# Kernel optimization log

Hardware: AMD Instinct MI355X
Metric: run time of the kernel (lower is better)

## Reference

```python
import jax, jax.numpy as jnp
import numpy as np

N_NODES = 100000
N_EDGES = 1600000
D_IN = 64
HID = 64


def setup_inputs() -> dict:
    key = jax.random.key(0)
    ks = jax.random.split(key, 8)
    s = 0.1  # modest weight scale
    return {
        "x": jax.random.normal(ks[0], (N_NODES, D_IN), jnp.float32),
        "edge_index": jax.random.randint(ks[1], (2, N_EDGES), 0, N_NODES),
        "W1": jax.random.normal(ks[2], (D_IN, HID), jnp.float32) * s,
        "b1": jnp.zeros((HID,), jnp.float32),
        "W2": jax.random.normal(ks[3], (HID, HID), jnp.float32) * s,
        "b2": jnp.zeros((HID,), jnp.float32),
        "fc1_w": jax.random.normal(ks[4], (HID, 256), jnp.float32) * s,
        "fc1_b": jnp.zeros((256,), jnp.float32),
        "fc2_w": jax.random.normal(ks[5], (256, 1), jnp.float32) * s,
        "fc2_b": jnp.zeros((1,), jnp.float32),
    }


def reference(x, edge_index, W1, b1, W2, b2, fc1_w, fc1_b, fc2_w, fc2_b):
    N = x.shape[0]
    loop = jnp.arange(N, dtype=edge_index.dtype)
    # GCNConv default: add self-loops + symmetric D^{-1/2}(A+I)D^{-1/2} normalization
    row = jnp.concatenate([edge_index[0], loop])  # source nodes
    col = jnp.concatenate([edge_index[1], loop])  # target nodes
    deg = jax.ops.segment_sum(jnp.ones(row.shape[0], x.dtype), col, num_segments=N)
    dinv = jnp.where(deg > 0, jax.lax.rsqrt(deg), 0.0)
    norm = dinv[row] * dinv[col]  # [E+N]

    def gcn_conv(h, W, b):
        h = h @ W                                   # [N, H] transform first
        msg = h[row] * norm[:, None]                # gather + scale, [E+N, H]
        return jax.ops.segment_sum(msg, col, num_segments=N) + b

    # dropout is inactive in eval mode (training=False)
    h = jax.nn.relu(gcn_conv(x, W1, b1))
    h = jax.nn.relu(gcn_conv(h, W2, b2))
    h = jax.nn.relu(h @ fc1_w + fc1_b)
    out = h @ fc2_w + fc2_b                          # [N, 1]
    # F.normalize(out, dim=0): L2 normalize along node dim, eps=1e-12
    out = out / jnp.maximum(jnp.sqrt(jnp.sum(out * out, axis=0, keepdims=True)), 1e-12)
    return out
```

## Files before the change

### kernel.cpp

```cpp
#include <hip/hip_runtime.h>
#include <hip/hip_bf16.h>

typedef unsigned short u16;
typedef unsigned int u32;
typedef __attribute__((ext_vector_type(8))) short short8;
typedef __attribute__((ext_vector_type(4))) float f32x4;

__device__ __forceinline__ float bf2f(u16 h) {
  return __uint_as_float(((u32)h) << 16);
}
__device__ __forceinline__ float ldconv(const void* p, int i, int fl) {
  return fl ? bf2f(((const u16*)p)[i]) : ((const float*)p)[i];
}
__device__ __forceinline__ u16 f2bf(float v) {
  __hip_bfloat16 h = __float2bfloat16(v);
  return *(u16*)&h;
}

__global__ void k_flag(const void* x, int* flag, float* ssum, int* bcnt) {
  __shared__ float red[256];
  int t = threadIdx.x;
  const u16* h = (const u16*)x;
  float m = 0.f;
  for (int i = t; i < 1024; i += 256) m = fmaxf(m, fabsf(bf2f(h[i])));
  red[t] = m; __syncthreads();
  for (int off = 128; off > 0; off >>= 1) {
    if (t < off) red[t] = fmaxf(red[t], red[t + off]);
    __syncthreads();
  }
  bcnt[t] = 0;
  if (t == 0) { *flag = (red[0] < 1000.0f) ? 1 : 0; *ssum = 0.f; }
}

__global__ void k_conv_w(const void* W1, const void* b1, const void* W2, const void* b2,
                         const void* f1w, const void* f1b, const void* f2w, const void* f2b,
                         u16* wbh, float* wbf, const int* flag) {
  int fl = *flag;
  int i = blockIdx.x * blockDim.x + threadIdx.x;
  if (i < 4096) {
    int n = i >> 6, k = i & 63;
    wbh[i] = f2bf(ldconv(W1, k * 64 + n, fl));
  } else if (i < 8192) {
    int j = i - 4096; int n = j >> 6, k = j & 63;
    wbh[i] = f2bf(ldconv(W2, k * 64 + n, fl));
  } else if (i < 24576) {
    int j = i - 8192; int n = j >> 6, k = j & 63;
    wbh[i] = f2bf(ldconv(f1w, k * 256 + n, fl));
  } else if (i < 24576 + 641) {
    int j = i - 24576;
    float v;
    if (j < 64)       v = ldconv(b1,  j,       fl);
    else if (j < 128) v = ldconv(b2,  j - 64,  fl);
    else if (j < 384) v = ldconv(f1b, j - 128, fl);
    else if (j < 640) v = ldconv(f2w, j - 384, fl);
    else              v = ldconv(f2b, 0,       fl);
    wbf[j] = v;
  }
}

__global__ __launch_bounds__(256) void k_bcount(const int* __restrict__ eidx, int E, int npb,
                                                int* bcnt) {
  __shared__ int hist[256];
  int t = threadIdx.x;
  hist[t] = 0;
  __syncthreads();
  int e0 = blockIdx.x * 8192;
  int e1 = min(e0 + 8192, E);
  for (int e = e0 + t; e < e1; e += 256) {
    int tgt = eidx[E + e];
    atomicAdd(&hist[tgt / npb], 1);
  }
  __syncthreads();
  if (hist[t]) atomicAdd(&bcnt[t], hist[t]);
}

__global__ void k_bscan(const int* __restrict__ bcnt, int* bbase, int* bcur) {
  __shared__ int tmp[256];
  int t = threadIdx.x;
  int v = bcnt[t];
  tmp[t] = v; __syncthreads();
  for (int off = 1; off < 256; off <<= 1) {
    int u = (t >= off) ? tmp[t - off] : 0;
    __syncthreads();
    tmp[t] += u;
    __syncthreads();
  }
  bbase[t] = tmp[t] - v;
  bcur[t]  = tmp[t] - v;
}

__global__ __launch_bounds__(256) void k_bfill(const int* __restrict__ eidx, int E, int npb,
                                               int* bcur, u32* bdata) {
  __shared__ int hist[256];
  __shared__ int base[256];
  int t = threadIdx.x;
  hist[t] = 0;
  __syncthreads();
  int e0 = blockIdx.x * 8192;
  int e1 = min(e0 + 8192, E);
  for (int e = e0 + t; e < e1; e += 256) {
    int tgt = eidx[E + e];
    atomicAdd(&hist[tgt / npb], 1);
  }
  __syncthreads();
  base[t] = hist[t] ? atomicAdd(&bcur[t], hist[t]) : 0;
  hist[t] = 0;
  __syncthreads();
  for (int e = e0 + t; e < e1; e += 256) {
    int src = eidx[e];
    int tgt = eidx[E + e];
    int b = tgt / npb;
    int idx = atomicAdd(&hist[b], 1);
    bdata[base[b] + idx] = ((u32)src << 9) | (u32)(tgt - b * npb);
  }
}

__global__ __launch_bounds__(256) void k_degb(const u32* __restrict__ bdata,
                                              const int* __restrict__ bbase,
                                              const int* __restrict__ bcnt,
                                              int* deg, int N, int npb) {
  __shared__ int hist[512];
  int b = blockIdx.x, t = threadIdx.x;
  int node0 = b * npb;
  if (node0 >= N) return;
  int ncnt = min(npb, N - node0);
  for (int j = t; j < 512; j += 256) hist[j] = 0;
  __syncthreads();
  int base = bbase[b], cnt = bcnt[b];
  for (int e = t; e < cnt; e += 256) atomicAdd(&hist[bdata[base + e] & 511], 1);
  __syncthreads();
  for (int j = t; j < ncnt; j += 256) deg[node0 + j] = hist[j] + 1;
}

__global__ void k_scan_a(const int* __restrict__ deg, int* csr_ptr, int* bsum, int N) {
  __shared__ int tmp[256];
  int t = threadIdx.x;
  int i = blockIdx.x * 256 + t;
  int c = (i < N) ? (deg[i] - 1) : 0;
  tmp[t] = c; __syncthreads();
  for (int off = 1; off < 256; off <<= 1) {
    int u = (t >= off) ? tmp[t - off] : 0;
    __syncthreads();
    tmp[t] += u;
    __syncthreads();
  }
  if (i < N) csr_ptr[i] = tmp[t] - c;
  if (t == 255) bsum[blockIdx.x] = tmp[255];
}

__global__ void k_scan_b(const int* __restrict__ bsum, int* bsum2, int G) {
  __shared__ int tmp[512];
  int t = threadIdx.x;
  int v = (t < G) ? bsum[t] : 0;
  tmp[t] = v; __syncthreads();
  for (int off = 1; off < 512; off <<= 1) {
    int u = (t >= off) ? tmp[t - off] : 0;
    __syncthreads();
    tmp[t] += u;
    __syncthreads();
  }
  if (t < G) bsum2[t] = tmp[t] - v;
}

__global__ void k_scan_c(int* csr_ptr, const int* __restrict__ bsum2,
                         const int* __restrict__ deg, float* dinv, int N) {
  int i = blockIdx.x * 256 + threadIdx.x;
  if (i >= N) return;
  csr_ptr[i] += bsum2[blockIdx.x];
  dinv[i] = 1.0f / sqrtf((float)deg[i]);
}

__global__ __launch_bounds__(256) void k_p2(const u32* __restrict__ bdata,
                                            const int* __restrict__ bbase,
                                            const int* __restrict__ bcnt,
                                            const int* __restrict__ csr_ptr,
                                            int* __restrict__ crow, int N, int npb, int E) {
  __shared__ int lds[8192];
  __shared__ int cur[512];
  int b = blockIdx.x, t = threadIdx.x;
  int node0 = b * npb;
  if (node0 >= N) return;
  int ncnt = min(npb, N - node0);
  int rs = csr_ptr[node0];
  int re = (node0 + ncnt < N) ? csr_ptr[node0 + ncnt] : E;
  for (int j = t; j < ncnt; j += 256) cur[j] = csr_ptr[node0 + j] - rs;
  __syncthreads();
  int base = bbase[b], cnt = bcnt[b];
  for (int e = t; e < cnt; e += 256) {
    u32 pk = bdata[base + e];
    int tl = pk & 511;
    int pos = atomicAdd(&cur[tl], 1);
    if (pos < 8192) lds[pos] = (int)(pk >> 9);
  }
  __syncthreads();
  int len = re - rs;
  for (int j = t; j < len; j += 256) crow[rs + j] = lds[j];
}

__global__ __launch_bounds__(256) void k_xform(const void* __restrict__ in, int inbf,
                                               const int* __restrict__ flagp,
                                               const u16* __restrict__ wT,
                                               const float* __restrict__ dinv,
                                               u16* __restrict__ out, int N) {
  __shared__ __align__(16) u16 ws[64 * 72];
  int t = threadIdx.x;
  #pragma unroll
  for (int f = t; f < 512; f += 256) {
    int n = f >> 3, o = f & 7;
    *(float4*)&ws[n * 72 + o * 8] = ((const float4*)wT)[f];
  }
  __syncthreads();
  int fl = inbf ? 1 : *flagp;
  int lane = t & 63, wid = t >> 6;
  int g = lane >> 4, c = lane & 15;
  int arow = blockIdx.x * 64 + wid * 16 + c;
  short8 a0 = {0, 0, 0, 0, 0, 0, 0, 0}, a1 = {0, 0, 0, 0, 0, 0, 0, 0};
  if (arow < N) {
    if (fl) {
      const u16* p = (const u16*)in + (size_t)arow * 64 + g * 8;
      a0 = *(const short8*)p;
      a1 = *(const short8*)(p + 32);
    } else {
      const float* p = (const float*)in + (size_t)arow * 64 + g * 8;
      u16 tmp[16];
      #pragma unroll
      for (int j = 0; j < 8; j++) tmp[j] = f2bf(p[j]);
      #pragma unroll
      for (int j = 0; j < 8; j++) tmp[8 + j] = f2bf(p[32 + j]);
      a0 = *(short8*)tmp;
      a1 = *(short8*)(tmp + 8);
    }
  }
  int rbase = blockIdx.x * 64 + wid * 16 + g * 4;
  float dv[4];
  #pragma unroll
  for (int r = 0; r < 4; r++) dv[r] = (rbase + r < N) ? dinv[rbase + r] : 0.f;
  #pragma unroll
  for (int tile = 0; tile < 4; tile++) {
    short8 b0 = *(const short8*)&ws[(tile * 16 + c) * 72 + g * 8];
    short8 b1 = *(const short8*)&ws[(tile * 16 + c) * 72 + g * 8 + 32];
    f32x4 z = {0.f, 0.f, 0.f, 0.f};
    f32x4 acc = __builtin_amdgcn_mfma_f32_16x16x32_bf16(a0, b0, z, 0, 0, 0);
    acc = __builtin_amdgcn_mfma_f32_16x16x32_bf16(a1, b1, acc, 0, 0, 0);
    #pragma unroll
    for (int r = 0; r < 4; r++) {
      int orow = rbase + r;
      if (orow < N) out[(size_t)orow * 64 + tile * 16 + c] = f2bf(acc[r] * dv[r]);
    }
  }
}

__global__ __launch_bounds__(256) void k_agg(const u16* __restrict__ src, u16* __restrict__ dst,
                                             const int* __restrict__ csr_row,
                                             const int* __restrict__ csr_ptr,
                                             const int* __restrict__ deg,
                                             const float* __restrict__ dinv,
                                             const float* __restrict__ bias, int N) {
  int lane = threadIdx.x & 63;
  int wid = threadIdx.x >> 6;
  int i = blockIdx.x * 4 + wid;
  if (i >= N) return;
  int sub = lane >> 4;
  int fq  = lane & 15;
  int start = csr_ptr[i];
  int total = deg[i];
  const u16* base = src + (size_t)fq * 4;
  float a0 = 0.f, a1 = 0.f, a2 = 0.f, a3 = 0.f;
  #pragma unroll 2
  for (int t = sub; t < total; t += 4) {
    int r = (t == 0) ? i : csr_row[start + t - 1];
    uint2 v = *(const uint2*)(base + (size_t)r * 64);
    a0 += __uint_as_float(v.x << 16);
    a1 += __uint_as_float(v.x & 0xffff0000u);
    a2 += __uint_as_float(v.y << 16);
    a3 += __uint_as_float(v.y & 0xffff0000u);
  }
  a0 += __shfl_xor(a0, 16); a1 += __shfl_xor(a1, 16);
  a2 += __shfl_xor(a2, 16); a3 += __shfl_xor(a3, 16);
  a0 += __shfl_xor(a0, 32); a1 += __shfl_xor(a1, 32);
  a2 += __shfl_xor(a2, 32); a3 += __shfl_xor(a3, 32);
  if (sub == 0) {
    float di = dinv[i];
    float4 b4 = ((const float4*)bias)[fq];
    u16 o[4];
    o[0] = f2bf(fmaxf(fmaf(a0, di, b4.x), 0.f));
    o[1] = f2bf(fmaxf(fmaf(a1, di, b4.y), 0.f));
    o[2] = f2bf(fmaxf(fmaf(a2, di, b4.z), 0.f));
    o[3] = f2bf(fmaxf(fmaf(a3, di, b4.w), 0.f));
    *(uint2*)&dst[(size_t)i * 64 + fq * 4] = *(uint2*)o;
  }
}

__global__ __launch_bounds__(256) void k_fc(const u16* __restrict__ h,
                                            const u16* __restrict__ fc1T,
                                            const float* __restrict__ wf,
                                            float* __restrict__ outf,
                                            float* __restrict__ ssum, int N) {
  __shared__ __align__(16) u16 ws[256 * 72];
  __shared__ float red[16];
  int t = threadIdx.x;
  #pragma unroll
  for (int f = t; f < 2048; f += 256) {
    int n = f >> 3, o = f & 7;
    *(float4*)&ws[n * 72 + o * 8] = ((const float4*)fc1T)[f];
  }
  __syncthreads();
  int lane = t & 63, wid = t >> 6;
  int g = lane >> 4, c = lane & 15;
  int arow = blockIdx.x * 64 + wid * 16 + c;
  short8 a0 = {0, 0, 0, 0, 0, 0, 0, 0}, a1 = {0, 0, 0, 0, 0, 0, 0, 0};
  if (arow < N) {
    a0 = *(const short8*)&h[(size_t)arow * 64 + g * 8];
    a1 = *(const short8*)&h[(size_t)arow * 64 + g * 8 + 32];
  }
  float psum[4] = {0.f, 0.f, 0.f, 0.f};
  #pragma unroll
  for (int tile = 0; tile < 16; tile++) {
    short8 b0 = *(const short8*)&ws[(tile * 16 + c) * 72 + g * 8];
    short8 b1 = *(const short8*)&ws[(tile * 16 + c) * 72 + g * 8 + 32];
    f32x4 z = {0.f, 0.f, 0.f, 0.f};
    f32x4 acc = __builtin_amdgcn_mfma_f32_16x16x32_bf16(a0, b0, z, 0, 0, 0);
    acc = __builtin_amdgcn_mfma_f32_16x16x32_bf16(a1, b1, acc, 0, 0, 0);
    int col = tile * 16 + c;
    float fb = wf[128 + col];
    float fw = wf[384 + col];
    #pragma unroll
    for (int r = 0; r < 4; r++) psum[r] += fmaxf(acc[r] + fb, 0.f) * fw;
  }
  #pragma unroll
  for (int off = 1; off < 16; off <<= 1) {
    #pragma unroll
    for (int r = 0; r < 4; r++) psum[r] += __shfl_xor(psum[r], off);
  }
  float fc2b = wf[640];
  if (c == 0) {
    float ss = 0.f;
    int rbase = blockIdx.x * 64 + wid * 16 + g * 4;
    #pragma unroll
    for (int r = 0; r < 4; r++) {
      int row = rbase + r;
      if (row < N) {
        float o = psum[r] + fc2b;
        outf[row] = o;
        ss += o * o;
      }
    }
    red[wid * 4 + g] = ss;
  }
  __syncthreads();
  if (t == 0) {
    float s = 0.f;
    #pragma unroll
    for (int j = 0; j < 16; j++) s += red[j];
    atomicAdd(ssum, s);
  }
}

__global__ void k_norm(const float* __restrict__ outf, const float* __restrict__ ssum,
                       void* dout, int N, const int* flag) {
  int i = blockIdx.x * blockDim.x + threadIdx.x;
  if (i >= N) return;
  float denom = fmaxf(sqrtf(*ssum), 1e-12f);
  float v = outf[i] / denom;
  if (*flag) ((__hip_bfloat16*)dout)[i] = __float2bfloat16(v);
  else       ((float*)dout)[i] = v;
}

extern "C" void kernel_launch(void* const* d_in, const int* in_sizes, int n_in,
                              void* d_out, int out_size, void* d_ws, size_t ws_size,
                              hipStream_t stream) {
  const void* x   = d_in[0];
  const int* eidx = (const int*)d_in[1];
  const void* W1  = d_in[2]; const void* b1  = d_in[3];
  const void* W2  = d_in[4]; const void* b2  = d_in[5];
  const void* f1w = d_in[6]; const void* f1b = d_in[7];
  const void* f2w = d_in[8]; const void* f2b = d_in[9];
  int N = in_sizes[0] / 64;
  int E = in_sizes[1] / 2;
  int npb = (N + 255) / 256;

  char* ws = (char*)d_ws;
  size_t off = 0;
  auto alloc = [&](size_t b) {
    void* p = ws + off;
    off = (off + b + 255) & ~(size_t)255;
    return p;
  };
  int*   flag  = (int*)  alloc(4);
  float* ssum  = (float*)alloc(4);
  int*   bcnt  = (int*)  alloc(256 * 4);
  int*   bbase = (int*)  alloc(256 * 4);
  int*   bcur  = (int*)  alloc(256 * 4);
  u32*   bdata = (u32*)  alloc((size_t)E * 4);
  int*   deg   = (int*)  alloc((size_t)N * 4);
  int*   ptr   = (int*)  alloc((size_t)N * 4);
  int*   bsum  = (int*)  alloc(512 * 4);
  int*   bsum2 = (int*)  alloc(512 * 4);
  float* dinv  = (float*)alloc((size_t)N * 4);
  int*   crow  = (int*)  alloc((size_t)E * 4);
  u16*   wbh   = (u16*)  alloc(24576 * 2);
  float* wbf   = (float*)alloc(641 * 4);
  u16*   HA    = (u16*)  alloc((size_t)N * 64 * 2);
  u16*   HT    = (u16*)  alloc((size_t)N * 64 * 2);
  float* outf  = (float*)alloc((size_t)N * 4);

  int GN = (N + 255) / 256;
  int GEB = (E + 8191) / 8192;
  int NT = (N + 63) / 64;

  k_flag<<<1, 256, 0, stream>>>(x, flag, ssum, bcnt);
  k_conv_w<<<(24576 + 641 + 255) / 256, 256, 0, stream>>>(W1, b1, W2, b2, f1w, f1b, f2w, f2b,
                                                          wbh, wbf, flag);
  k_bcount<<<GEB, 256, 0, stream>>>(eidx, E, npb, bcnt);
  k_bscan<<<1, 256, 0, stream>>>(bcnt, bbase, bcur);
  k_bfill<<<GEB, 256, 0, stream>>>(eidx, E, npb, bcur, bdata);
  k_degb<<<256, 256, 0, stream>>>(bdata, bbase, bcnt, deg, N, npb);
  k_scan_a<<<GN, 256, 0, stream>>>(deg, ptr, bsum, N);
  k_scan_b<<<1, 512, 0, stream>>>(bsum, bsum2, GN);
  k_scan_c<<<GN, 256, 0, stream>>>(ptr, bsum2, deg, dinv, N);
  k_p2<<<256, 256, 0, stream>>>(bdata, bbase, bcnt, ptr, crow, N, npb, E);

  k_xform<<<NT, 256, 0, stream>>>(x, 0, flag, wbh + 0, dinv, HT, N);
  k_agg<<<(N + 3) / 4, 256, 0, stream>>>(HT, HA, crow, ptr, deg, dinv, wbf + 0, N);
  k_xform<<<NT, 256, 0, stream>>>(HA, 1, flag, wbh + 4096, dinv, HT, N);
  k_agg<<<(N + 3) / 4, 256, 0, stream>>>(HT, HA, crow, ptr, deg, dinv, wbf + 64, N);
  k_fc<<<NT, 256, 0, stream>>>(HA, wbh + 8192, wbf, outf, ssum, N);
  k_norm<<<GN, 256, 0, stream>>>(outf, ssum, d_out, N, flag);
}
```

Measured before the change: 318.4 us.

## Restructure CSR build into 256-node buckets with fused degree/scan/fill kernel

```diff
diff --git a/kernel.cpp b/kernel.cpp
--- a/kernel.cpp
+++ b/kernel.cpp
@@ -28,7 +28,7 @@
     if (t < off) red[t] = fmaxf(red[t], red[t + off]);
     __syncthreads();
   }
-  bcnt[t] = 0;
+  bcnt[t] = 0; bcnt[t + 256] = 0;
   if (t == 0) { *flag = (red[0] < 1000.0f) ? 1 : 0; *ssum = 0.f; }
 }
 
@@ -58,143 +58,103 @@
   }
 }
 
-__global__ __launch_bounds__(256) void k_bcount(const int* __restrict__ eidx, int E, int npb,
-                                                int* bcnt) {
-  __shared__ int hist[256];
-  int t = threadIdx.x;
-  hist[t] = 0;
+__global__ __launch_bounds__(256) void k_bcount(const int* __restrict__ eidx, int E,
+                                                int* bcnt, int* blockhist) {
+  __shared__ int hist[512];
+  int t = threadIdx.x;
+  hist[t] = 0; hist[t + 256] = 0;
+  __syncthreads();
+  int e0 = blockIdx.x * 8192;
+  int e1 = min(e0 + 8192, E);
+  for (int e = e0 + t; e < e1; e += 256) atomicAdd(&hist[eidx[E + e] >> 8], 1);
+  __syncthreads();
+  int* bh = blockhist + blockIdx.x * 512;
+  for (int j = t; j < 512; j += 256) {
+    bh[j] = hist[j];
+    if (hist[j]) atomicAdd(&bcnt[j], hist[j]);
+  }
+}
+
+__global__ void k_bscan(const int* __restrict__ bcnt, int* bbase, int* bcur) {
+  __shared__ int tmp[512];
+  int t = threadIdx.x;
+  int v = bcnt[t];
+  tmp[t] = v; __syncthreads();
+  for (int off = 1; off < 512; off <<= 1) {
+    int u = (t >= off) ? tmp[t - off] : 0;
+    __syncthreads();
+    tmp[t] += u;
+    __syncthreads();
+  }
+  bbase[t] = tmp[t] - v;
+  bcur[t]  = tmp[t] - v;
+}
+
+__global__ __launch_bounds__(256) void k_bfill(const int* __restrict__ eidx, int E,
+                                               const int* __restrict__ blockhist,
+                                               int* bcur, u32* bdata) {
+  __shared__ int base[512];
+  __shared__ int hist[512];
+  int t = threadIdx.x;
+  const int* bh = blockhist + blockIdx.x * 512;
+  for (int j = t; j < 512; j += 256) {
+    int c = bh[j];
+    base[j] = c ? atomicAdd(&bcur[j], c) : 0;
+    hist[j] = 0;
+  }
   __syncthreads();
   int e0 = blockIdx.x * 8192;
   int e1 = min(e0 + 8192, E);
   for (int e = e0 + t; e < e1; e += 256) {
+    int src = eidx[e];
     int tgt = eidx[E + e];
-    atomicAdd(&hist[tgt / npb], 1);
-  }
-  __syncthreads();
-  if (hist[t]) atomicAdd(&bcnt[t], hist[t]);
-}
-
-__global__ void k_bscan(const int* __restrict__ bcnt, int* bbase, int* bcur) {
+    int b = tgt >> 8;
+    int idx = atomicAdd(&hist[b], 1);
+    bdata[base[b] + idx] = ((u32)src << 8) | (u32)(tgt & 255);
+  }
+}
+
+__global__ __launch_bounds__(256) void k_csr(const u32* __restrict__ bdata,
+                                             const int* __restrict__ bbase,
+                                             const int* __restrict__ bcnt,
+                                             int* __restrict__ deg, float* __restrict__ dinv,
+                                             int* __restrict__ ptr, int* __restrict__ crow,
+                                             int N) {
+  __shared__ int lds[8192];
+  __shared__ int hist[256];
   __shared__ int tmp[256];
-  int t = threadIdx.x;
-  int v = bcnt[t];
-  tmp[t] = v; __syncthreads();
+  __shared__ int cur[256];
+  int b = blockIdx.x, t = threadIdx.x;
+  int node0 = b << 8;
+  int ncnt = min(256, N - node0);
+  hist[t] = 0;
+  __syncthreads();
+  int base = bbase[b], cnt = bcnt[b];
+  for (int e = t; e < cnt; e += 256) atomicAdd(&hist[bdata[base + e] & 255], 1);
+  __syncthreads();
+  int h = hist[t];
+  if (t < ncnt) {
+    deg[node0 + t] = h + 1;
+    dinv[node0 + t] = 1.0f / sqrtf((float)(h + 1));
+  }
+  tmp[t] = h; __syncthreads();
   for (int off = 1; off < 256; off <<= 1) {
     int u = (t >= off) ? tmp[t - off] : 0;
     __syncthreads();
     tmp[t] += u;
     __syncthreads();
   }
-  bbase[t] = tmp[t] - v;
-  bcur[t]  = tmp[t] - v;
-}
-
-__global__ __launch_bounds__(256) void k_bfill(const int* __restrict__ eidx, int E, int npb,
-                                               int* bcur, u32* bdata) {
-  __shared__ int hist[256];
-  __shared__ int base[256];
-  int t = threadIdx.x;
-  hist[t] = 0;
-  __syncthreads();
-  int e0 = blockIdx.x * 8192;
-  int e1 = min(e0 + 8192, E);
-  for (int e = e0 + t; e < e1; e += 256) {
-    int tgt = eidx[E + e];
-    atomicAdd(&hist[tgt / npb], 1);
-  }
-  __syncthreads();
-  base[t] = hist[t] ? atomicAdd(&bcur[t], hist[t]) : 0;
-  hist[t] = 0;
-  __syncthreads();
-  for (int e = e0 + t; e < e1; e += 256) {
-    int src = eidx[e];
-    int tgt = eidx[E + e];
-    int b = tgt / npb;
-    int idx = atomicAdd(&hist[b], 1);
-    bdata[base[b] + idx] = ((u32)src << 9) | (u32)(tgt - b * npb);
-  }
-}
-
-__global__ __launch_bounds__(256) void k_degb(const u32* __restrict__ bdata,
-                                              const int* __restrict__ bbase,
-                                              const int* __restrict__ bcnt,
-                                              int* deg, int N, int npb) {
-  __shared__ int hist[512];
-  int b = blockIdx.x, t = threadIdx.x;
-  int node0 = b * npb;
-  if (node0 >= N) return;
-  int ncnt = min(npb, N - node0);
-  for (int j = t; j < 512; j += 256) hist[j] = 0;
-  __syncthreads();
-  int base = bbase[b], cnt = bcnt[b];
-  for (int e = t; e < cnt; e += 256) atomicAdd(&hist[bdata[base + e] & 511], 1);
-  __syncthreads();
-  for (int j = t; j < ncnt; j += 256) deg[node0 + j] = hist[j] + 1;
-}
-
-__global__ void k_scan_a(const int* __restrict__ deg, int* csr_ptr, int* bsum, int N) {
-  __shared__ int tmp[256];
-  int t = threadIdx.x;
-  int i = blockIdx.x * 256 + t;
-  int c = (i < N) ? (deg[i] - 1) : 0;
-  tmp[t] = c; __syncthreads();
-  for (int off = 1; off < 256; off <<= 1) {
-    int u = (t >= off) ? tmp[t - off] : 0;
-    __syncthreads();
-    tmp[t] += u;
-    __syncthreads();
-  }
-  if (i < N) csr_ptr[i] = tmp[t] - c;
-  if (t == 255) bsum[blockIdx.x] = tmp[255];
-}
-
-__global__ void k_scan_b(const int* __restrict__ bsum, int* bsum2, int G) {
-  __shared__ int tmp[512];
-  int t = threadIdx.x;
-  int v = (t < G) ? bsum[t] : 0;
-  tmp[t] = v; __syncthreads();
-  for (int off = 1; off < 512; off <<= 1) {
-    int u = (t >= off) ? tmp[t - off] : 0;
-    __syncthreads();
-    tmp[t] += u;
-    __syncthreads();
-  }
-  if (t < G) bsum2[t] = tmp[t] - v;
-}
-
-__global__ void k_scan_c(int* csr_ptr, const int* __restrict__ bsum2,
-                         const int* __restrict__ deg, float* dinv, int N) {
-  int i = blockIdx.x * 256 + threadIdx.x;
-  if (i >= N) return;
-  csr_ptr[i] += bsum2[blockIdx.x];
-  dinv[i] = 1.0f / sqrtf((float)deg[i]);
-}
-
-__global__ __launch_bounds__(256) void k_p2(const u32* __restrict__ bdata,
-                                            const int* __restrict__ bbase,
-                                            const int* __restrict__ bcnt,
-                                            const int* __restrict__ csr_ptr,
-                                            int* __restrict__ crow, int N, int npb, int E) {
-  __shared__ int lds[8192];
-  __shared__ int cur[512];
-  int b = blockIdx.x, t = threadIdx.x;
-  int node0 = b * npb;
-  if (node0 >= N) return;
-  int ncnt = min(npb, N - node0);
-  int rs = csr_ptr[node0];
-  int re = (node0 + ncnt < N) ? csr_ptr[node0 + ncnt] : E;
-  for (int j = t; j < ncnt; j += 256) cur[j] = csr_ptr[node0 + j] - rs;
-  __syncthreads();
-  int base = bbase[b], cnt = bcnt[b];
+  int excl = tmp[t] - h;
+  if (t < ncnt) ptr[node0 + t] = base + excl;
+  cur[t] = excl;
+  __syncthreads();
   for (int e = t; e < cnt; e += 256) {
     u32 pk = bdata[base + e];
-    int tl = pk & 511;
-    int pos = atomicAdd(&cur[tl], 1);
-    if (pos < 8192) lds[pos] = (int)(pk >> 9);
-  }
-  __syncthreads();
-  int len = re - rs;
-  for (int j = t; j < len; j += 256) crow[rs + j] = lds[j];
+    int pos = atomicAdd(&cur[pk & 255], 1);
+    if (pos < 8192) lds[pos] = (int)(pk >> 8);
+  }
+  __syncthreads();
+  for (int j = t; j < cnt; j += 256) crow[base + j] = lds[j];
 }
 
 __global__ __launch_bounds__(256) void k_xform(const void* __restrict__ in, int inbf,
@@ -222,13 +182,13 @@
       a1 = *(const short8*)(p + 32);
     } else {
       const float* p = (const float*)in + (size_t)arow * 64 + g * 8;
-      u16 tmp[16];
+      u16 tmpv[16];
       #pragma unroll
-      for (int j = 0; j < 8; j++) tmp[j] = f2bf(p[j]);
+      for (int j = 0; j < 8; j++) tmpv[j] = f2bf(p[j]);
       #pragma unroll
-      for (int j = 0; j < 8; j++) tmp[8 + j] = f2bf(p[32 + j]);
-      a0 = *(short8*)tmp;
-      a1 = *(short8*)(tmp + 8);
+      for (int j = 0; j < 8; j++) tmpv[8 + j] = f2bf(p[32 + j]);
+      a0 = *(short8*)tmpv;
+      a1 = *(short8*)(tmpv + 8);
     }
   }
   int rbase = blockIdx.x * 64 + wid * 16 + g * 4;
@@ -266,7 +226,7 @@
   int total = deg[i];
   const u16* base = src + (size_t)fq * 4;
   float a0 = 0.f, a1 = 0.f, a2 = 0.f, a3 = 0.f;
-  #pragma unroll 2
+  #pragma unroll 4
   for (int t = sub; t < total; t += 4) {
     int r = (t == 0) ? i : csr_row[start + t - 1];
     uint2 v = *(const uint2*)(base + (size_t)r * 64);
@@ -377,7 +337,8 @@
   const void* f2w = d_in[8]; const void* f2b = d_in[9];
   int N = in_sizes[0] / 64;
   int E = in_sizes[1] / 2;
-  int npb = (N + 255) / 256;
+  int NB = (N + 255) >> 8;
+  int GEB = (E + 8191) / 8192;
 
   char* ws = (char*)d_ws;
   size_t off = 0;
@@ -388,14 +349,13 @@
   };
   int*   flag  = (int*)  alloc(4);
   float* ssum  = (float*)alloc(4);
-  int*   bcnt  = (int*)  alloc(256 * 4);
-  int*   bbase = (int*)  alloc(256 * 4);
-  int*   bcur  = (int*)  alloc(256 * 4);
+  int*   bcnt  = (int*)  alloc(512 * 4);
+  int*   bbase = (int*)  alloc(512 * 4);
+  int*   bcur  = (int*)  alloc(512 * 4);
+  int*   bhist = (int*)  alloc((size_t)GEB * 512 * 4);
   u32*   bdata = (u32*)  alloc((size_t)E * 4);
   int*   deg   = (int*)  alloc((size_t)N * 4);
   int*   ptr   = (int*)  alloc((size_t)N * 4);
-  int*   bsum  = (int*)  alloc(512 * 4);
-  int*   bsum2 = (int*)  alloc(512 * 4);
   float* dinv  = (float*)alloc((size_t)N * 4);
   int*   crow  = (int*)  alloc((size_t)E * 4);
   u16*   wbh   = (u16*)  alloc(24576 * 2);
@@ -405,20 +365,15 @@
   float* outf  = (float*)alloc((size_t)N * 4);
 
   int GN = (N + 255) / 256;
-  int GEB = (E + 8191) / 8192;
   int NT = (N + 63) / 64;
 
   k_flag<<<1, 256, 0, stream>>>(x, flag, ssum, bcnt);
   k_conv_w<<<(24576 + 641 + 255) / 256, 256, 0, stream>>>(W1, b1, W2, b2, f1w, f1b, f2w, f2b,
                                                           wbh, wbf, flag);
-  k_bcount<<<GEB, 256, 0, stream>>>(eidx, E, npb, bcnt);
-  k_bscan<<<1, 256, 0, stream>>>(bcnt, bbase, bcur);
-  k_bfill<<<GEB, 256, 0, stream>>>(eidx, E, npb, bcur, bdata);
-  k_degb<<<256, 256, 0, stream>>>(bdata, bbase, bcnt, deg, N, npb);
-  k_scan_a<<<GN, 256, 0, stream>>>(deg, ptr, bsum, N);
-  k_scan_b<<<1, 512, 0, stream>>>(bsum, bsum2, GN);
-  k_scan_c<<<GN, 256, 0, stream>>>(ptr, bsum2, deg, dinv, N);
-  k_p2<<<256, 256, 0, stream>>>(bdata, bbase, bcnt, ptr, crow, N, npb, E);
+  k_bcount<<<GEB, 256, 0, stream>>>(eidx, E, bcnt, bhist);
+  k_bscan<<<1, 512, 0, stream>>>(bcnt, bbase, bcur);
+  k_bfill<<<GEB, 256, 0, stream>>>(eidx, E, bhist, bcur, bdata);
+  k_csr<<<NB, 256, 0, stream>>>(bdata, bbase, bcnt, deg, dinv, ptr, crow, N);
 
   k_xform<<<NT, 256, 0, stream>>>(x, 0, flag, wbh + 0, dinv, HT, N);
   k_agg<<<(N + 3) / 4, 256, 0, stream>>>(HT, HA, crow, ptr, deg, dinv, wbf + 0, N);
```

After: 295.1 us. -7.3%, faster.
